# Optimization experiments

Measured on AMD Instinct MI355X. Metric: run time of the kernel, lower is better.

Reference implementation:

```python
import jax, jax.numpy as jnp
import numpy as np

FEAT_STRIDE = 8
SCALES = (4.0, 8.0, 16.0)
RATIOS = (0.5, 1.0, 2.0)
A = len(SCALES) * len(RATIOS)          # 9 anchors per location
PRE_NMS = 2048
POST_NMS = 300
NMS_THRESH = 0.7


def _gen_base_anchors():
    # cube anchors at scale*stride, ratio applied to depth; boxes (x1,y1,z1,x2,y2,z2)
    base = float(FEAT_STRIDE)
    ctr = (base - 1.0) / 2.0
    boxes = []
    for r in RATIOS:
        for s in SCALES:
            w = h = base * s
            d = base * s * r
            boxes.append([ctr - 0.5 * (w - 1), ctr - 0.5 * (h - 1), ctr - 0.5 * (d - 1),
                          ctr + 0.5 * (w - 1), ctr + 0.5 * (h - 1), ctr + 0.5 * (d - 1)])
    return jnp.asarray(boxes, jnp.float32)  # [A,6]


def _all_anchors(D, H, W):
    sz = jnp.arange(D, dtype=jnp.float32) * FEAT_STRIDE
    sy = jnp.arange(H, dtype=jnp.float32) * FEAT_STRIDE
    sx = jnp.arange(W, dtype=jnp.float32) * FEAT_STRIDE
    zz, yy, xx = jnp.meshgrid(sz, sy, sx, indexing='ij')  # order (d,h,w) matches score layout
    shifts = jnp.stack([xx, yy, zz, xx, yy, zz], -1).reshape(-1, 6)  # [K,6]
    return (shifts[:, None, :] + _gen_base_anchors()[None]).reshape(-1, 6)  # [K*A,6]


def _apply_deltas(anchors, deltas):
    w = anchors[:, 3] - anchors[:, 0] + 1.0
    h = anchors[:, 4] - anchors[:, 1] + 1.0
    d = anchors[:, 5] - anchors[:, 2] + 1.0
    cx = anchors[:, 0] + 0.5 * w
    cy = anchors[:, 1] + 0.5 * h
    cz = anchors[:, 2] + 0.5 * d
    dx, dy, dz, dw, dh, dd = [deltas[:, i] for i in range(6)]
    pcx = dx * w + cx; pcy = dy * h + cy; pcz = dz * d + cz
    pw = jnp.exp(dw) * w; ph = jnp.exp(dh) * h; pd = jnp.exp(dd) * d
    return jnp.stack([pcx - 0.5 * pw, pcy - 0.5 * ph, pcz - 0.5 * pd,
                      pcx + 0.5 * pw, pcy + 0.5 * ph, pcz + 0.5 * pd], -1)


def _clip_boxes(boxes, iminfo):  # iminfo = [D_im, H_im, W_im]
    lo = jnp.zeros((6,), boxes.dtype)
    hi = jnp.stack([iminfo[2], iminfo[1], iminfo[0], iminfo[2], iminfo[1], iminfo[0]]) - 1.0
    return jnp.clip(boxes, lo[None, :], hi[None, :])


def _pairwise_iou3d(b):  # b: [N,6]
    lo = jnp.maximum(b[:, None, :3], b[None, :, :3])          # [N,N,3]
    hi = jnp.minimum(b[:, None, 3:], b[None, :, 3:])
    inter = jnp.prod(jnp.clip(hi - lo + 1.0, 0.0), axis=-1)   # [N,N]
    vol = jnp.prod(b[:, 3:] - b[:, :3] + 1.0, axis=-1)        # [N]
    return inter / (vol[:, None] + vol[None, :] - inter)


def _nms_keep(iou):
    N = iou.shape[0]
    idx = jnp.arange(N)
    def body(i, keep):
        sup = (iou[i] > NMS_THRESH) & keep[i] & (idx > i)
        return keep & ~sup
    return jax.lax.fori_loop(0, N, body, jnp.ones((N,), bool))


def _propose_one(scores, deltas, anchors, iminfo):
    boxes = _clip_boxes(_apply_deltas(anchors, deltas), iminfo)  # [KA,6]
    _, order = jax.lax.top_k(scores, PRE_NMS)
    b = boxes[order]                                             # [PRE,6], score-sorted desc
    keep = _nms_keep(_pairwise_iou3d(b))
    key = jnp.where(keep, jnp.arange(PRE_NMS), PRE_NMS)
    sel = jnp.argsort(key)[:POST_NMS]                            # first POST_NMS kept, in score order
    valid = (key[sel] < PRE_NMS).astype(b.dtype)
    return b[sel] * valid[:, None]                               # zero-padded rows if < POST_NMS kept


def _forward(base_feat, im_info, W_conv, b_conv, W_cls, b_cls, W_bbox, b_bbox):
    B, C, D, H, W = base_feat.shape
    x = jax.lax.conv_general_dilated(
        base_feat, W_conv, (1, 1, 1), ((1, 1), (1, 1), (1, 1)),
        dimension_numbers=('NCDHW', 'OIDHW', 'NCDHW'))
    x = jax.nn.relu(x + b_conv[None, :, None, None, None])       # [B,512,D,H,W]
    cls = jnp.einsum('bcdhw,oc->bodhw', x, W_cls) + b_cls[None, :, None, None, None]
    prob = jax.nn.softmax(cls.reshape(B, 2, A, D, H, W), axis=1)  # reshape(x,2) + softmax(dim=1)
    fg = prob[:, 1]                                               # [B,A,D,H,W]
    scores = jnp.transpose(fg, (0, 2, 3, 4, 1)).reshape(B, -1)    # [B, K*A], order (d,h,w,a)
    bb = jnp.einsum('bcdhw,oc->bodhw', x, W_bbox) + b_bbox[None, :, None, None, None]
    deltas = jnp.transpose(bb.reshape(B, A, 6, D, H, W), (0, 3, 4, 5, 1, 2)).reshape(B, -1, 6)
    anchors = _all_anchors(D, H, W)
    rois6 = jax.vmap(lambda s, d, im: _propose_one(s, d, anchors, im))(scores, deltas, im_info)
    bidx = jnp.broadcast_to(jnp.arange(B, dtype=rois6.dtype)[:, None, None], (B, POST_NMS, 1))
    return jnp.concatenate([bidx, rois6], -1)                     # [B, POST_NMS, 7]


def setup_inputs() -> dict:
    key = jax.random.key(0)
    ks = jax.random.split(key, 4)
    B, din, D, H, W = 2, 128, 8, 32, 32
    base_feat = jax.random.normal(ks[0], (B, din, D, H, W), jnp.float32)
    im_info = jnp.asarray([[64.0, 256.0, 256.0]] * B, jnp.float32)  # (D_im, H_im, W_im)
    gt_boxes = jnp.zeros((B, 20, 7), jnp.float32)
    num_boxes = jnp.zeros((B,), jnp.int64)
    W_conv = jax.random.normal(ks[1], (512, din, 3, 3, 3), jnp.float32) * 0.02
    b_conv = jnp.zeros((512,), jnp.float32)
    W_cls = jax.random.normal(ks[2], (2 * A, 512), jnp.float32) * 0.01
    b_cls = jnp.zeros((2 * A,), jnp.float32)
    W_bbox = jax.random.normal(ks[3], (6 * A, 512), jnp.float32) * 0.01
    b_bbox = jnp.zeros((6 * A,), jnp.float32)
    return {"base_feat": base_feat, "im_info": im_info, "gt_boxes": gt_boxes,
            "num_boxes": num_boxes, "W_conv": W_conv, "b_conv": b_conv,
            "W_cls": W_cls, "b_cls": b_cls, "W_bbox": W_bbox, "b_bbox": b_bbox}


def reference(base_feat, im_info, gt_boxes, num_boxes, W_conv, b_conv, W_cls, b_cls, W_bbox, b_bbox):
    # Eval-mode RPN forward: losses are 0 in the original; gt_boxes/num_boxes unused.
    rois = _forward(base_feat, im_info, W_conv, b_conv, W_cls, b_cls, W_bbox, b_bbox)
    return rois
```

## Files before the change

kernel.cpp:

```cpp
#include <hip/hip_runtime.h>
#include <stdint.h>

#define BATCH 2
#define CIN 128
#define COUT 512
#define DD 8
#define PSPAT 8192
#define NA 9
#define NANCH 73728
#define PRE 2048
#define POST 300
#define CAP 4096
#define NMS_TH 0.7f

typedef unsigned short u16;
typedef _Float16 f16x8 __attribute__((ext_vector_type(8)));
typedef float f32x16 __attribute__((ext_vector_type(16)));
typedef unsigned int uint32x4 __attribute__((ext_vector_type(4)));

constexpr size_t OFF_WT   = 0;
constexpr size_t OFF_WHT  = 7077888;
constexpr size_t OFF_X    = 7241728;
constexpr size_t OFF_SC   = 40796160;
constexpr size_t OFF_BX   = 41385984;
constexpr size_t OFF_SB   = 44957696;
constexpr size_t OFF_MK   = 45056000;
constexpr size_t OFF_HIST = 16;
constexpr size_t OFF_XH   = 46104576;
constexpr size_t OFF_XL   = 50298880;

#define NT_WT   (27 * 128 * 512)
#define NT_WHT  (512 * 80)
__global__ void k_wtrans(const float* __restrict__ Wc, u16* __restrict__ Wg,
                         const float* __restrict__ Wcls, const float* __restrict__ Wbb,
                         float* __restrict__ Wht) {
    int e = blockIdx.x * blockDim.x + threadIdx.x;
    if (e < NT_WT) {
        const int k    = e & 63;
        const int n    = (e >> 6) & 63;
        const int half = (e >> 12) & 1;
        const int rest = e >> 13;
        const int co = (rest / 27) * 64 + n;
        const int ci = half * 64 + k;
        const int tp = rest % 27;
        const float v = Wc[(co * 128 + ci) * 27 + tp] * 1024.f;
        const _Float16 h = (_Float16)v;
        const _Float16 l = (_Float16)(v - (float)h);
        char* rb = (char*)Wg + (((size_t)(rest * 2 + half)) << 14) + n * 256;
        const int hcol = (k >> 3) ^ (n & 15);
        const int lcol = ((k >> 3) | 8) ^ (n & 15);
        const int kb = (k & 7) << 1;
        *(u16*)(rb + (hcol << 4) + kb) = __builtin_bit_cast(unsigned short, h);
        *(u16*)(rb + (lcol << 4) + kb) = __builtin_bit_cast(unsigned short, l);
        return;
    }
    e -= NT_WT;
    if (e >= NT_WHT) return;
    int q = e % 80;
    int c = e / 80;
    int og = q / 10, k = q % 10;
    int o = og * 9 + k;
    float v = 0.f;
    if (k < 9) v = (o < 18) ? Wcls[o * 512 + c] : Wbb[(o - 18) * 512 + c];
    Wht[e] = v;
}

__global__ __launch_bounds__(256) void k_split(const float* __restrict__ in,
                                               u16* __restrict__ xh, u16* __restrict__ xl) {
    __shared__ float t[128][33];
    const int blk = blockIdx.x;
    const int b = blk >> 8, d = (blk >> 5) & 7, h = blk & 31;
    const int tid = threadIdx.x;
    const float* src = in + ((size_t)b << 20) + d * 1024 + h * 32;
    #pragma unroll
    for (int i = 0; i < 16; ++i) {
        const int e = tid + i * 256;
        const int ci = e >> 5, w = e & 31;
        t[ci][w] = src[(size_t)ci * 8192 + w];
    }
    __syncthreads();
    const size_t ob = (size_t)((b * 8 + d) * 32 + h) * 4096;
    #pragma unroll
    for (int i = 0; i < 2; ++i) {
        const int e = tid + i * 256;
        const int oct = e >> 5, w = e & 31;
        unsigned sh0, sh1, sh2, sh3, sl0, sl1, sl2, sl3;
        #define SPL2(C, SH, SL) { \
            const float va_ = t[oct * 8 + 2*(C)][w] * 1024.f; \
            const float vb_ = t[oct * 8 + 2*(C)+1][w] * 1024.f; \
            const _Float16 ha_ = (_Float16)va_, hb_ = (_Float16)vb_; \
            const _Float16 la_ = (_Float16)(va_ - (float)ha_); \
            const _Float16 lb_ = (_Float16)(vb_ - (float)hb_); \
            SH = (unsigned)__builtin_bit_cast(unsigned short, ha_) | \
                 ((unsigned)__builtin_bit_cast(unsigned short, hb_) << 16); \
            SL = (unsigned)__builtin_bit_cast(unsigned short, la_) | \
                 ((unsigned)__builtin_bit_cast(unsigned short, lb_) << 16); }
        SPL2(0, sh0, sl0) SPL2(1, sh1, sl1) SPL2(2, sh2, sl2) SPL2(3, sh3, sl3)
        #undef SPL2
        uint32x4 vh = {sh0, sh1, sh2, sh3};
        uint32x4 vl = {sl0, sl1, sl2, sl3};
        *(uint32x4*)(xh + ob + (size_t)e * 8) = vh;
        *(uint32x4*)(xl + ob + (size_t)e * 8) = vl;
    }
}

#define MFMA(A, B, C) __builtin_amdgcn_mfma_f32_32x32x16_f16((A), (B), (C), 0, 0, 0)
#define Z16 {0.f,0.f,0.f,0.f,0.f,0.f,0.f,0.f,0.f,0.f,0.f,0.f,0.f,0.f,0.f,0.f}

#define WISSUE(S, BUF) { \
    const int tap_ = t0 + ((S) >> 1); \
    const char* gw_ = WgB + (((size_t)((nt * 27 + tap_) * 2 + ((S) & 1))) << 14) \
                    + (wv << 13) + ln16; \
    char* lb_ = smem + ((BUF) << 14) + (wv << 13); \
    _Pragma("unroll") \
    for (int j_ = 0; j_ < 8; ++j_) \
        __builtin_amdgcn_global_load_lds( \
            (const __attribute__((address_space(1))) void*)(gw_ + (j_ << 10)), \
            (__attribute__((address_space(3))) void*)(lb_ + (j_ << 10)), 16, 0, 0); }

#define KKSTEP(KK, BH0, BL0, BH1, BL1) { \
    const int ch_ = ((((KK) << 1) + cq) ^ rsw) << 4; \
    const int cl_ = (((((KK) << 1) + cq) | 8) ^ rsw) << 4; \
    const char* r0_ = wb_ + (rm0 << 8); \
    const char* r1_ = wb_ + (rm1 << 8); \
    const f16x8 wh0 = *(const f16x8*)(r0_ + ch_); \
    const f16x8 wl0 = *(const f16x8*)(r0_ + cl_); \
    const f16x8 wh1 = *(const f16x8*)(r1_ + ch_); \
    const f16x8 wl1 = *(const f16x8*)(r1_ + cl_); \
    acc00 = MFMA(wh0, BH0, acc00); \
    acc01 = MFMA(wh0, BH1, acc01); \
    acc10 = MFMA(wh1, BH0, acc10); \
    acc11 = MFMA(wh1, BH1, acc11); \
    acc00 = MFMA(wh0, BL0, acc00); \
    acc01 = MFMA(wh0, BL1, acc01); \
    acc10 = MFMA(wh1, BL0, acc10); \
    acc11 = MFMA(wh1, BL1, acc11); \
    acc00 = MFMA(wl0, BH0, acc00); \
    acc01 = MFMA(wl0, BH1, acc01); \
    acc10 = MFMA(wl1, BH0, acc10); \
    acc11 = MFMA(wl1, BH1, acc11); }

#define EPI(ACC, MI, NI) { \
    const int coB_ = co0 + ((MI) << 5) + hl4; \
    const int pt_  = p0 + (wn << 6) + ((NI) << 5) + l31; \
    _Pragma("unroll") \
    for (int g_ = 0; g_ < 4; ++g_) { \
        _Pragma("unroll") \
        for (int q_ = 0; q_ < 4; ++q_) { \
            const int co_ = coB_ + (g_ << 3) + q_; \
            const float v_ = ACC[g_ * 4 + q_] * 9.5367431640625e-07f + bconv[co_]; \
            x[((size_t)((b << 9) + co_) << 13) + pt_] = fmaxf(v_, 0.f); \
        } } }

#define FLD(N, KK, BH, BL) { \
    const int h2_ = hb_ + (N); \
    const bool ok_ = okw_ && ((unsigned)h2_ < 32u); \
    const size_t ix_ = sbase_ + ((size_t)(h2_ & 31) << 12); \
    const f16x8 vh_ = *(const f16x8*)(xh + ix_ + ((KK) << 9)); \
    const f16x8 vl_ = *(const f16x8*)(xl + ix_ + ((KK) << 9)); \
    BH = ok_ ? vh_ : fz8; \
    BL = ok_ ? vl_ : fz8; }

#define ALOADF(S, P) { \
    const int tap_ = t0 + ((S) >> 1); \
    const int kd_ = tap_ / 9, kh_ = (tap_ / 3) % 3, kw_ = tap_ % 3; \
    const int id_ = d0 + kd_ - 1; \
    const int w2_ = l31 + kw_ - 1; \
    const bool okw_ = (unsigned)w2_ < 32u; \
    const int hb_ = h0 + (wn << 1) + kh_ - 1; \
    const int oc0_ = (((S) & 1) << 3) + cq; \
    const size_t sbase_ = (((size_t)((b << 3) + id_)) << 17) + (oc0_ << 8) + ((w2_ & 31) << 3); \
    FLD(0, 0, P##h00, P##l00) FLD(0, 1, P##h01, P##l01) \
    FLD(0, 2, P##h02, P##l02) FLD(0, 3, P##h03, P##l03) \
    FLD(1, 0, P##h10, P##l10) FLD(1, 1, P##h11, P##l11) \
    FLD(1, 2, P##h12, P##l12) FLD(1, 3, P##h13, P##l13) }

#define COMPUTEF(BUF, P) { \
    const char* wb_ = smem + ((BUF) << 14); \
    __builtin_amdgcn_s_setprio(1); \
    KKSTEP(0, P##h00, P##l00, P##h10, P##l10) \
    KKSTEP(1, P##h01, P##l01, P##h11, P##l11) \
    KKSTEP(2, P##h02, P##l02, P##h12, P##l12) \
    KKSTEP(3, P##h03, P##l03, P##h13, P##l13) \
    __builtin_amdgcn_s_setprio(0); }

#define VMCNT24 asm volatile("s_waitcnt vmcnt(24)" ::: "memory");
#define VMCNT16 asm volatile("s_waitcnt vmcnt(16)" ::: "memory");
#define VMCNT0  asm volatile("s_waitcnt vmcnt(0)"  ::: "memory");
#define SBAR    __builtin_amdgcn_s_barrier();
#define SCHED0  __builtin_amdgcn_sched_barrier(0);

__global__ __launch_bounds__(128, 2) void k_conv_f(const u16* __restrict__ xh,
                                                   const u16* __restrict__ xl,
                                                   const u16* __restrict__ Wg,
                                                   const float* __restrict__ bconv,
                                                   float* __restrict__ x) {
    __shared__ __align__(16) char smem[32768];
    const int tid  = threadIdx.x;
    const int bx   = blockIdx.x;
    const int nt   = blockIdx.y;
    const int b    = blockIdx.z;
    const int p0   = bx << 7;
    const int d0   = bx >> 3;
    const int h0   = (bx & 7) << 2;
    const int co0  = nt << 6;

    const int lane = tid & 63;
    const int wv   = tid >> 6;
    const int wn   = wv;
    const int l31  = lane & 31;
    const int cq   = lane >> 5;
    const int hl4  = cq << 2;
    const int rsw  = l31 & 15;
    const int rm0  = l31;
    const int rm1  = l31 + 32;
    const int ln16 = lane << 4;

    const int t0   = (d0 == 0) ? 9 : 0;
    const int nTap = 27 - (((d0 == 0) || (d0 == 7)) ? 9 : 0);
    const int NS   = nTap * 2;

    const char* WgB = (const char*)Wg;
    const f16x8 fz8 = {(_Float16)0.f, (_Float16)0.f, (_Float16)0.f, (_Float16)0.f,
                       (_Float16)0.f, (_Float16)0.f, (_Float16)0.f, (_Float16)0.f};

    f16x8 Ah00, Al00, Ah01, Al01, Ah02, Al02, Ah03, Al03,
          Ah10, Al10, Ah11, Al11, Ah12, Al12, Ah13, Al13;
    f16x8 Bh00, Bl00, Bh01, Bl01, Bh02, Bl02, Bh03, Bl03,
          Bh10, Bl10, Bh11, Bl11, Bh12, Bl12, Bh13, Bl13;
    f32x16 acc00 = Z16, acc01 = Z16, acc10 = Z16, acc11 = Z16;

    WISSUE(0, 0)
    SCHED0
    ALOADF(0, A)
    VMCNT16
    SBAR

    for (int s = 0; s < NS; s += 2) {
        WISSUE(s + 1, 1)
        SCHED0
        ALOADF(s + 1, B)
        VMCNT24
        SCHED0
        COMPUTEF(0, A)
        VMCNT16
        SBAR
        if (s + 2 < NS) {
            WISSUE(s + 2, 0)
            SCHED0
            ALOADF(s + 2, A)
            VMCNT24
        } else {
            VMCNT0
        }
        SCHED0
        COMPUTEF(1, B)
        if (s + 2 < NS) {
            VMCNT16
            SBAR
        }
    }

    EPI(acc00, 0, 0)
    EPI(acc01, 0, 1)
    EPI(acc10, 1, 0)
    EPI(acc11, 1, 1)
}

__global__ __launch_bounds__(256) void k_heads(const float* __restrict__ x,
                                               const float* __restrict__ Wht,
                                               const float* __restrict__ bcls,
                                               const float* __restrict__ bbb,
                                               const float* __restrict__ iminfo,
                                               float* __restrict__ scores,
                                               float* __restrict__ boxes,
                                               unsigned int* __restrict__ hist) {
    __shared__ __align__(16) float smx[2048];
    __shared__ __align__(16) float Whs[2560];
    __shared__ __align__(16) float ex[5120];
    const int tid = threadIdx.x;
    const int p0  = blockIdx.x * 64;
    const int b   = blockIdx.y;
    const int pl  = tid & 31;
    const int og  = tid >> 5;

    float acc[2][9] = {};

    for (int cc = 0; cc < 512; cc += 32) {
        __syncthreads();
        #pragma unroll
        for (int i = 0; i < 2; ++i) {
            int e4 = tid + i * 256;
            int ch = e4 >> 4;
            int pt4 = (e4 & 15) * 4;
            *(float4*)&smx[ch * 64 + pt4] =
                *(const float4*)&x[((size_t)(b * COUT + cc + ch) << 13) + p0 + pt4];
        }
        #pragma unroll
        for (int i = 0; i < 10; ++i) {
            int e = tid + i * 256;
            Whs[e] = Wht[cc * 80 + e];
        }
        __syncthreads();
        for (int kk = 0; kk < 32; ++kk) {
            float2 a2 = *(const float2*)&smx[kk * 64 + pl * 2];
            const float* wp = &Whs[kk * 80 + og * 10];
            float2 w0 = *(const float2*)(wp);
            float2 w1 = *(const float2*)(wp + 2);
            float2 w2 = *(const float2*)(wp + 4);
            float2 w3 = *(const float2*)(wp + 6);
            float  w8 = wp[8];
            float wv[9] = {w0.x, w0.y, w1.x, w1.y, w2.x, w2.y, w3.x, w3.y, w8};
            #pragma unroll
            for (int k = 0; k < 9; ++k) {
                float wk = wv[k];
                acc[0][k] += a2.x * wk;
                acc[1][k] += a2.y * wk;
            }
        }
    }

    __syncthreads();
    #pragma unroll
    for (int pi = 0; pi < 2; ++pi)
        #pragma unroll
        for (int k = 0; k < 9; ++k)
            ex[(pl * 2 + pi) * 80 + og * 10 + k] = acc[pi][k];
    __syncthreads();

    if (tid < 64) {
        const int p = p0 + tid;
        float v[72];
        #pragma unroll
        for (int og2 = 0; og2 < 8; ++og2)
            #pragma unroll
            for (int k = 0; k < 9; ++k)
                v[og2 * 9 + k] = ex[tid * 80 + og2 * 10 + k];

        const float im0 = iminfo[b * 3 + 0], im1 = iminfo[b * 3 + 1], im2 = iminfo[b * 3 + 2];
        const float hix = im2 - 1.f, hiy = im1 - 1.f, hiz = im0 - 1.f;
        const int d = p >> 10, h = (p >> 5) & 31, w = p & 31;
        const float sx = w * 8.f, sy = h * 8.f, sz = d * 8.f;

        #pragma unroll 1
        for (int a = 0; a < 9; ++a) {
            float c0 = v[a] + bcls[a];
            float c1 = v[9 + a] + bcls[9 + a];
            float m  = fmaxf(c0, c1);
            float e0 = expf(c0 - m), e1 = expf(c1 - m);
            float sc = e1 / (e0 + e1);
            scores[b * NANCH + p * 9 + a] = sc;
            atomicAdd(&hist[b * 65536 + (__float_as_uint(sc) >> 16)], 1u);

            float aw = (float)(32 << (a % 3));
            float ad = aw * 0.5f * (float)(1 << (a / 3));
            float ax1 = sx + 3.5f - 0.5f * (aw - 1.f);
            float ax2 = sx + 3.5f + 0.5f * (aw - 1.f);
            float ay1 = sy + 3.5f - 0.5f * (aw - 1.f);
            float ay2 = sy + 3.5f + 0.5f * (aw - 1.f);
            float az1 = sz + 3.5f - 0.5f * (ad - 1.f);
            float az2 = sz + 3.5f + 0.5f * (ad - 1.f);
            float ww_ = ax2 - ax1 + 1.f, hh_ = ay2 - ay1 + 1.f, dd_ = az2 - az1 + 1.f;
            float cx = ax1 + 0.5f * ww_, cy = ay1 + 0.5f * hh_, cz = az1 + 0.5f * dd_;

            const float* dv = &v[18 + a * 6];
            float dx = dv[0] + bbb[a * 6 + 0];
            float dy = dv[1] + bbb[a * 6 + 1];
            float dz = dv[2] + bbb[a * 6 + 2];
            float dw = dv[3] + bbb[a * 6 + 3];
            float dh = dv[4] + bbb[a * 6 + 4];
            float dd2 = dv[5] + bbb[a * 6 + 5];
            float pcx = dx * ww_ + cx, pcy = dy * hh_ + cy, pcz = dz * dd_ + cz;
            float pw = expf(dw) * ww_, ph = expf(dh) * hh_, pd = expf(dd2) * dd_;
            float x1 = fminf(fmaxf(pcx - 0.5f * pw, 0.f), hix);
            float y1 = fminf(fmaxf(pcy - 0.5f * ph, 0.f), hiy);
            float z1 = fminf(fmaxf(pcz - 0.5f * pd, 0.f), hiz);
            float x2 = fminf(fmaxf(pcx + 0.5f * pw, 0.f), hix);
            float y2 = fminf(fmaxf(pcy + 0.5f * ph, 0.f), hiy);
            float z2 = fminf(fmaxf(pcz + 0.5f * pd, 0.f), hiz);
            float* bp = &boxes[(size_t)(b * NANCH + p * 9 + a) * 6];
            bp[0] = x1; bp[1] = y1; bp[2] = z1; bp[3] = x2; bp[4] = y2; bp[5] = z2;
        }
    }
}

__global__ __launch_bounds__(1024) void k_select(const float* __restrict__ scores,
                                                 const unsigned int* __restrict__ hist,
                                                 const float* __restrict__ boxes,
                                                 float* __restrict__ sboxes) {
    __shared__ unsigned int cs[1024], scan[1024];
    __shared__ unsigned int sh_cut, sh_pos;
    __shared__ unsigned long long sk[CAP];
    const int b = blockIdx.x, tid = threadIdx.x;
    const unsigned int* h = hist + b * 65536;
    unsigned int s = 0;
    for (int i = 0; i < 64; ++i) s += h[tid * 64 + i];
    cs[tid] = s; scan[tid] = s;
    if (tid == 0) sh_pos = 0;
    __syncthreads();
    for (int d = 1; d < 1024; d <<= 1) {
        unsigned int v = scan[tid];
        unsigned int add = (tid + d < 1024) ? scan[tid + d] : 0u;
        __syncthreads();
        scan[tid] = v + add;
        __syncthreads();
    }
    unsigned int above = (tid + 1 < 1024) ? scan[tid + 1] : 0u;
    if (above < PRE && above + cs[tid] >= PRE) {
        unsigned int cum = above;
        for (int x = tid * 64 + 63; x >= tid * 64; --x) {
            cum += h[x];
            if (cum >= PRE) { sh_cut = (unsigned int)x; break; }
        }
    }
    __syncthreads();
    const unsigned int cut = sh_cut;
    const float* sc = scores + b * NANCH;
    for (int i = tid; i < NANCH; i += 1024) {
        unsigned int u = __float_as_uint(sc[i]);
        if ((u >> 16) >= cut) {
            unsigned int pos = atomicAdd(&sh_pos, 1u);
            if (pos < CAP) sk[pos] = ((unsigned long long)(~u) << 32) | (unsigned)i;
        }
    }
    __syncthreads();
    const unsigned int cnt = (sh_pos < CAP) ? sh_pos : CAP;
    for (int i = (int)cnt + tid; i < CAP; i += 1024)
        sk[i] = ~0ull;
    __syncthreads();
    for (int k = 2; k <= CAP; k <<= 1) {
        for (int j = k >> 1; j > 0; j >>= 1) {
            #pragma unroll 1
            for (int i = tid; i < CAP; i += 1024) {
                int ixj = i ^ j;
                if (ixj > i) {
                    unsigned long long va = sk[i], vb = sk[ixj];
                    bool up = ((i & k) == 0);
                    if ((va > vb) == up) { sk[i] = vb; sk[ixj] = va; }
                }
            }
            __syncthreads();
        }
    }
    for (int r = tid; r < PRE; r += 1024) {
        unsigned int n = (unsigned int)(sk[r] & 0xFFFFFFFFull);
        const float* src = &boxes[(size_t)(b * NANCH + (int)n) * 6];
        float* dst = &sboxes[(size_t)(b * PRE + r) * 6];
        #pragma unroll
        for (int c = 0; c < 6; ++c) dst[c] = src[c];
    }
}

__global__ __launch_bounds__(256) void k_mask(const float* __restrict__ sboxes,
                                              unsigned long long* __restrict__ mask) {
    if (blockIdx.y < blockIdx.x) return;
    __shared__ float rb[64 * 6], cb[64 * 6];
    const int i0 = blockIdx.x * 64, j0 = blockIdx.y * 64, b = blockIdx.z;
    const int tid = threadIdx.x;
    for (int e = tid; e < 384; e += 256) {
        rb[e] = sboxes[(size_t)(b * PRE + i0) * 6 + e];
        cb[e] = sboxes[(size_t)(b * PRE + j0) * 6 + e];
    }
    __syncthreads();
    const int wave = tid >> 6, lane = tid & 63;
    const float bx1 = cb[lane * 6 + 0], by1 = cb[lane * 6 + 1], bz1 = cb[lane * 6 + 2];
    const float bx2 = cb[lane * 6 + 3], by2 = cb[lane * 6 + 4], bz2 = cb[lane * 6 + 5];
    const float vb = (bx2 - bx1 + 1.f) * (by2 - by1 + 1.f) * (bz2 - bz1 + 1.f);
    const int j = j0 + lane;
    for (int rr = 0; rr < 16; ++rr) {
        const int il = wave * 16 + rr;
        const int i = i0 + il;
        float ax1 = rb[il * 6 + 0], ay1 = rb[il * 6 + 1], az1 = rb[il * 6 + 2];
        float ax2 = rb[il * 6 + 3], ay2 = rb[il * 6 + 4], az2 = rb[il * 6 + 5];
        float va = (ax2 - ax1 + 1.f) * (ay2 - ay1 + 1.f) * (az2 - az1 + 1.f);
        float ix = fmaxf(fminf(ax2, bx2) - fmaxf(ax1, bx1) + 1.f, 0.f);
        float iy = fmaxf(fminf(ay2, by2) - fmaxf(ay1, by1) + 1.f, 0.f);
        float iz = fmaxf(fminf(az2, bz2) - fmaxf(az1, bz1) + 1.f, 0.f);
        float inter = ix * iy * iz;
        float iou = inter / (va + vb - inter);
        bool bit = (j > i) && (iou > NMS_TH);
        unsigned long long word = __ballot(bit);
        if (lane == 0) mask[(size_t)(b * PRE + i) * 32 + (j0 >> 6)] = word;
    }
}

__global__ __launch_bounds__(64) void k_nms(const unsigned long long* __restrict__ mask,
                                            const float* __restrict__ sboxes,
                                            float* __restrict__ out) {
    const int b = blockIdx.x, lane = threadIdx.x;
    __shared__ int sel[POST];
    unsigned long long keep = ~0ull;
    const int lw = lane & 31;
    const unsigned long long* mrow = mask + (size_t)b * PRE * 32 + lw;
    unsigned long long b0 = mrow[0 * 32], b1 = mrow[1 * 32], b2 = mrow[2 * 32], b3 = mrow[3 * 32];
    unsigned long long b4 = mrow[4 * 32], b5 = mrow[5 * 32], b6 = mrow[6 * 32], b7 = mrow[7 * 32];
    int kcount = 0;

#define NMS_STEP(J, BUF)                                                        \
    {                                                                           \
        int i = i0 + (J);                                                       \
        unsigned long long cur = (lw >= (i >> 6)) ? BUF : 0ull;                 \
        int nr = i0 + 8 + (J);                                                  \
        BUF = (nr < PRE) ? mrow[(size_t)nr * 32] : 0ull;                        \
        unsigned long long kw = __shfl(keep, i >> 6);                           \
        if ((kw >> (i & 63)) & 1ull) {                                          \
            if (lane < 32) keep &= ~cur;                                        \
            if (lane == 0 && kcount < POST) sel[kcount] = i;                    \
            ++kcount;                                                           \
            if (kcount >= POST) goto nms_done;                                  \
        }                                                                       \
    }

    for (int i0 = 0; i0 < PRE; i0 += 8) {
        NMS_STEP(0, b0) NMS_STEP(1, b1) NMS_STEP(2, b2) NMS_STEP(3, b3)
        NMS_STEP(4, b4) NMS_STEP(5, b5) NMS_STEP(6, b6) NMS_STEP(7, b7)
    }
nms_done:
    __syncthreads();
    const int kc = kcount;
    for (int r = lane; r < POST; r += 64) {
        float* op = &out[(size_t)(b * POST + r) * 7];
        op[0] = (float)b;
        if (r < kc) {
            const float* sb = &sboxes[(size_t)(b * PRE + sel[r]) * 6];
            #pragma unroll
            for (int c = 0; c < 6; ++c) op[1 + c] = sb[c];
        } else {
            #pragma unroll
            for (int c = 0; c < 6; ++c) op[1 + c] = 0.f;
        }
    }
#undef NMS_STEP
}

extern "C" void kernel_launch(void* const* d_in, const int* in_sizes, int n_in,
                              void* d_out, int out_size, void* d_ws, size_t ws_size,
                              hipStream_t stream) {
    const float* base_feat = (const float*)d_in[0];
    const float* im_info   = (const float*)d_in[1];
    const float* W_conv    = (const float*)d_in[4];
    const float* b_conv    = (const float*)d_in[5];
    const float* W_cls     = (const float*)d_in[6];
    const float* b_cls     = (const float*)d_in[7];
    const float* W_bbox    = (const float*)d_in[8];
    const float* b_bbox    = (const float*)d_in[9];

    char* ws = (char*)d_ws;
    u16* Wg        = (u16*)(ws + OFF_WT);
    float* Wht     = (float*)(ws + OFF_WHT);
    float* x       = (float*)(ws + OFF_X);
    float* scores  = (float*)(ws + OFF_SC);
    float* boxes   = (float*)(ws + OFF_BX);
    float* sboxes  = (float*)(ws + OFF_SB);
    unsigned long long* mask = (unsigned long long*)(ws + OFF_MK);
    unsigned int* hist = (unsigned int*)(ws + OFF_HIST);
    u16* xh        = (u16*)(ws + OFF_XH);
    u16* xl        = (u16*)(ws + OFF_XL);

    const int NTRANS = NT_WT + NT_WHT;
    k_wtrans<<<(NTRANS + 255) / 256, 256, 0, stream>>>(W_conv, Wg, W_cls, W_bbox, Wht);
    k_split<<<512, 256, 0, stream>>>(base_feat, xh, xl);
    k_conv_f<<<dim3(64, 8, 2), 128, 0, stream>>>(xh, xl, Wg, b_conv, x);
    hipMemsetAsync(hist, 0, BATCH * 65536 * sizeof(unsigned int), stream);
    k_heads<<<dim3(128, 2), 256, 0, stream>>>(x, Wht, b_cls, b_bbox, im_info, scores, boxes, hist);
    k_select<<<BATCH, 1024, 0, stream>>>(scores, hist, boxes, sboxes);
    k_mask<<<dim3(32, 32, 2), 256, 0, stream>>>(sboxes, mask);
    k_nms<<<BATCH, 64, 0, stream>>>(mask, sboxes, (float*)d_out);
}
```

Baseline: 565.3 us.

## Fuse weight transform and input split into one prep kernel with LDS-staged stores

The separate weight-transform and input-split kernels are merged into a single launch that dispatches on block index. The conv weight repack now builds each 16 KB swizzled tile in shared memory and writes it out with 16-byte vector stores, replacing scattered 2-byte global writes. The histogram buffer is moved into the mask region so its memset can be issued before the prep kernel without clobbering the weights. Global reads of the conv weights remain strided.

```diff
diff --git a/kernel.cpp b/kernel.cpp
--- a/kernel.cpp
+++ b/kernel.cpp
@@ -25,83 +25,100 @@
 constexpr size_t OFF_BX   = 41385984;
 constexpr size_t OFF_SB   = 44957696;
 constexpr size_t OFF_MK   = 45056000;
-constexpr size_t OFF_HIST = 16;
+constexpr size_t OFF_HIST = OFF_MK;
 constexpr size_t OFF_XH   = 46104576;
 constexpr size_t OFF_XL   = 50298880;
 
-#define NT_WT   (27 * 128 * 512)
 #define NT_WHT  (512 * 80)
-__global__ void k_wtrans(const float* __restrict__ Wc, u16* __restrict__ Wg,
-                         const float* __restrict__ Wcls, const float* __restrict__ Wbb,
-                         float* __restrict__ Wht) {
-    int e = blockIdx.x * blockDim.x + threadIdx.x;
-    if (e < NT_WT) {
-        const int k    = e & 63;
-        const int n    = (e >> 6) & 63;
-        const int half = (e >> 12) & 1;
-        const int rest = e >> 13;
-        const int co = (rest / 27) * 64 + n;
-        const int ci = half * 64 + k;
-        const int tp = rest % 27;
-        const float v = Wc[(co * 128 + ci) * 27 + tp] * 1024.f;
-        const _Float16 h = (_Float16)v;
-        const _Float16 l = (_Float16)(v - (float)h);
-        char* rb = (char*)Wg + (((size_t)(rest * 2 + half)) << 14) + n * 256;
-        const int hcol = (k >> 3) ^ (n & 15);
-        const int lcol = ((k >> 3) | 8) ^ (n & 15);
-        const int kb = (k & 7) << 1;
-        *(u16*)(rb + (hcol << 4) + kb) = __builtin_bit_cast(unsigned short, h);
-        *(u16*)(rb + (lcol << 4) + kb) = __builtin_bit_cast(unsigned short, l);
+
+__global__ __launch_bounds__(256) void k_prep(const float* __restrict__ in,
+                                              u16* __restrict__ xh, u16* __restrict__ xl,
+                                              const float* __restrict__ Wc,
+                                              u16* __restrict__ Wg,
+                                              const float* __restrict__ Wcls,
+                                              const float* __restrict__ Wbb,
+                                              float* __restrict__ Wht) {
+    __shared__ __align__(16) char sm[17024];
+    const int bid = blockIdx.x;
+    const int tid = threadIdx.x;
+
+    if (bid < 512) {
+        float (*t)[33] = (float(*)[33])sm;
+        const int b = bid >> 8, d = (bid >> 5) & 7, h = bid & 31;
+        const float* src = in + ((size_t)b << 20) + d * 1024 + h * 32;
+        #pragma unroll
+        for (int i = 0; i < 16; ++i) {
+            const int e = tid + i * 256;
+            const int ci = e >> 5, w = e & 31;
+            t[ci][w] = src[(size_t)ci * 8192 + w];
+        }
+        __syncthreads();
+        const size_t ob = (size_t)((b * 8 + d) * 32 + h) * 4096;
+        #pragma unroll
+        for (int i = 0; i < 2; ++i) {
+            const int e = tid + i * 256;
+            const int oct = e >> 5, w = e & 31;
+            unsigned sh0, sh1, sh2, sh3, sl0, sl1, sl2, sl3;
+            #define SPL2(C, SH, SL) { \
+                const float va_ = t[oct * 8 + 2*(C)][w] * 1024.f; \
+                const float vb_ = t[oct * 8 + 2*(C)+1][w] * 1024.f; \
+                const _Float16 ha_ = (_Float16)va_, hb_ = (_Float16)vb_; \
+                const _Float16 la_ = (_Float16)(va_ - (float)ha_); \
+                const _Float16 lb_ = (_Float16)(vb_ - (float)hb_); \
+                SH = (unsigned)__builtin_bit_cast(unsigned short, ha_) | \
+                     ((unsigned)__builtin_bit_cast(unsigned short, hb_) << 16); \
+                SL = (unsigned)__builtin_bit_cast(unsigned short, la_) | \
+                     ((unsigned)__builtin_bit_cast(unsigned short, lb_) << 16); }
+            SPL2(0, sh0, sl0) SPL2(1, sh1, sl1) SPL2(2, sh2, sl2) SPL2(3, sh3, sl3)
+            #undef SPL2
+            uint32x4 vh = {sh0, sh1, sh2, sh3};
+            uint32x4 vl = {sl0, sl1, sl2, sl3};
+            *(uint32x4*)(xh + ob + (size_t)e * 8) = vh;
+            *(uint32x4*)(xl + ob + (size_t)e * 8) = vl;
+        }
         return;
     }
-    e -= NT_WT;
+
+    if (bid < 944) {
+        u16* img = (u16*)sm;
+        const int rb2  = bid - 512;
+        const int rest = rb2 >> 1;
+        const int half = rb2 & 1;
+        const int nt = rest / 27, tp = rest % 27;
+        const int n  = tid >> 2;
+        const int k0 = (tid & 3) << 4;
+        const int co = nt * 64 + n;
+        const float* src = Wc + ((size_t)(co * 128 + half * 64 + k0)) * 27 + tp;
+        #pragma unroll
+        for (int i = 0; i < 16; ++i) {
+            const int k = k0 + i;
+            const float v = src[i * 27] * 1024.f;
+            const _Float16 h = (_Float16)v;
+            const _Float16 l = (_Float16)(v - (float)h);
+            const int hcol = (k >> 3) ^ (n & 15);
+            const int lcol = ((k >> 3) | 8) ^ (n & 15);
+            img[n * 128 + hcol * 8 + (k & 7)] = __builtin_bit_cast(unsigned short, h);
+            img[n * 128 + lcol * 8 + (k & 7)] = __builtin_bit_cast(unsigned short, l);
+        }
+        __syncthreads();
+        u16* dst = Wg + (((size_t)(rest * 2 + half)) << 13);
+        #pragma unroll
+        for (int i = 0; i < 4; ++i) {
+            const int e = tid + i * 256;
+            *(uint32x4*)(dst + (size_t)e * 8) = *(const uint32x4*)(img + e * 8);
+        }
+        return;
+    }
+
+    const int e = (bid - 944) * 256 + tid;
     if (e >= NT_WHT) return;
-    int q = e % 80;
-    int c = e / 80;
-    int og = q / 10, k = q % 10;
-    int o = og * 9 + k;
+    const int q = e % 80;
+    const int c = e / 80;
+    const int og = q / 10, k = q % 10;
+    const int o = og * 9 + k;
     float v = 0.f;
     if (k < 9) v = (o < 18) ? Wcls[o * 512 + c] : Wbb[(o - 18) * 512 + c];
     Wht[e] = v;
-}
-
-__global__ __launch_bounds__(256) void k_split(const float* __restrict__ in,
-                                               u16* __restrict__ xh, u16* __restrict__ xl) {
-    __shared__ float t[128][33];
-    const int blk = blockIdx.x;
-    const int b = blk >> 8, d = (blk >> 5) & 7, h = blk & 31;
-    const int tid = threadIdx.x;
-    const float* src = in + ((size_t)b << 20) + d * 1024 + h * 32;
-    #pragma unroll
-    for (int i = 0; i < 16; ++i) {
-        const int e = tid + i * 256;
-        const int ci = e >> 5, w = e & 31;
-        t[ci][w] = src[(size_t)ci * 8192 + w];
-    }
-    __syncthreads();
-    const size_t ob = (size_t)((b * 8 + d) * 32 + h) * 4096;
-    #pragma unroll
-    for (int i = 0; i < 2; ++i) {
-        const int e = tid + i * 256;
-        const int oct = e >> 5, w = e & 31;
-        unsigned sh0, sh1, sh2, sh3, sl0, sl1, sl2, sl3;
-        #define SPL2(C, SH, SL) { \
-            const float va_ = t[oct * 8 + 2*(C)][w] * 1024.f; \
-            const float vb_ = t[oct * 8 + 2*(C)+1][w] * 1024.f; \
-            const _Float16 ha_ = (_Float16)va_, hb_ = (_Float16)vb_; \
-            const _Float16 la_ = (_Float16)(va_ - (float)ha_); \
-            const _Float16 lb_ = (_Float16)(vb_ - (float)hb_); \
-            SH = (unsigned)__builtin_bit_cast(unsigned short, ha_) | \
-                 ((unsigned)__builtin_bit_cast(unsigned short, hb_) << 16); \
-            SL = (unsigned)__builtin_bit_cast(unsigned short, la_) | \
-                 ((unsigned)__builtin_bit_cast(unsigned short, lb_) << 16); }
-        SPL2(0, sh0, sl0) SPL2(1, sh1, sl1) SPL2(2, sh2, sl2) SPL2(3, sh3, sl3)
-        #undef SPL2
-        uint32x4 vh = {sh0, sh1, sh2, sh3};
-        uint32x4 vl = {sl0, sl1, sl2, sl3};
-        *(uint32x4*)(xh + ob + (size_t)e * 8) = vh;
-        *(uint32x4*)(xl + ob + (size_t)e * 8) = vl;
-    }
 }
 
 #define MFMA(A, B, C) __builtin_amdgcn_mfma_f32_32x32x16_f16((A), (B), (C), 0, 0, 0)
@@ -557,11 +574,9 @@
     u16* xh        = (u16*)(ws + OFF_XH);
     u16* xl        = (u16*)(ws + OFF_XL);
 
-    const int NTRANS = NT_WT + NT_WHT;
-    k_wtrans<<<(NTRANS + 255) / 256, 256, 0, stream>>>(W_conv, Wg, W_cls, W_bbox, Wht);
-    k_split<<<512, 256, 0, stream>>>(base_feat, xh, xl);
+    hipMemsetAsync(hist, 0, BATCH * 65536 * sizeof(unsigned int), stream);
+    k_prep<<<1104, 256, 0, stream>>>(base_feat, xh, xl, W_conv, Wg, W_cls, W_bbox, Wht);
     k_conv_f<<<dim3(64, 8, 2), 128, 0, stream>>>(xh, xl, Wg, b_conv, x);
-    hipMemsetAsync(hist, 0, BATCH * 65536 * sizeof(unsigned int), stream);
     k_heads<<<dim3(128, 2), 256, 0, stream>>>(x, Wht, b_cls, b_bbox, im_info, scores, boxes, hist);
     k_select<<<BATCH, 1024, 0, stream>>>(scores, hist, boxes, sboxes);
     k_mask<<<dim3(32, 32, 2), 256, 0, stream>>>(sboxes, mask);
```

Result: no change. 567.2 us (+0.3%).
